# Kernel optimization log

Hardware: AMD Instinct MI355X
Metric: run time of the kernel (lower is better)

The kernel has to match this reference:

```python
import jax, jax.numpy as jnp
import numpy as np

TOP_K = 2


def setup_inputs() -> dict:
    key = jax.random.key(0)
    k1, k2, k3, k4 = jax.random.split(key, 4)
    B, S, H, I, E = 8, 2048, 768, 3072, 8
    x = jax.random.normal(k1, (B, S, H), dtype=jnp.float32)
    # kaiming_uniform-ish scale for weights
    router_w = jax.random.uniform(k2, (E, H), dtype=jnp.float32, minval=-1.0, maxval=1.0) * (1.0 / np.sqrt(H))
    up_w = jax.random.uniform(k3, (E, H, I), dtype=jnp.float32, minval=-1.0, maxval=1.0) * (1.0 / np.sqrt(H))
    down_w = jax.random.uniform(k4, (E, I, H), dtype=jnp.float32, minval=-1.0, maxval=1.0) * (1.0 / np.sqrt(I))
    return {"x": x, "router_w": router_w, "up_w": up_w, "down_w": down_w}


def reference(x, router_w, up_w, down_w):
    B, S, H = x.shape
    E = up_w.shape[0]
    T = B * S
    xf = x.reshape(T, H)
    # router: Linear(H -> E, bias=False) then softmax, top-k, renormalize
    logits = xf @ router_w.T                      # [T, E]
    probs = jax.nn.softmax(logits, axis=-1)
    top_w, top_i = jax.lax.top_k(probs, TOP_K)    # [T, K]
    top_w = top_w / jnp.sum(top_w, axis=-1, keepdims=True)
    # dense per-(token, expert) gate: zero for unselected experts
    gate = jnp.zeros((T, E), dtype=xf.dtype).at[jnp.arange(T)[:, None], top_i].add(top_w)
    # combine: sum_e gate[:, e] * down_e(gelu(up_e(x)))
    out = jnp.zeros_like(xf)
    for e in range(E):  # fixed small expert count; loop is structural, not over data dims
        h = jax.nn.gelu(xf @ up_w[e], approximate=False)   # exact GELU == torch F.gelu
        out = out + gate[:, e:e + 1] * (h @ down_w[e])
    return out.reshape(B, S, H)
```

## Files before the change

kernel.cpp:

```cpp
#include <hip/hip_runtime.h>

typedef short bf16x8 __attribute__((ext_vector_type(8)));
typedef float f32x4  __attribute__((ext_vector_type(4)));

#define T_TOK 16384
#define HD 768
#define ID 3072
#define NE 8
#define NT1MAX 136

__device__ __forceinline__ unsigned short f2bf(float f) {
    unsigned int u = __float_as_uint(f);
    unsigned int r = (u + 0x7FFFu + ((u >> 16) & 1u)) >> 16;
    return (unsigned short)r;
}

__device__ __forceinline__ void gload16(const void* g, void* l) {
    __builtin_amdgcn_global_load_lds(
        (const __attribute__((address_space(1))) void*)g,
        (__attribute__((address_space(3))) void*)l, 16, 0, 0);
}

__device__ __forceinline__ float gelu_f(float x) {
    float z = fabsf(x) * 0.70710678118f;
    float t = 1.0f / fmaf(0.3275911f, z, 1.0f);
    float p = t * fmaf(t, fmaf(t, fmaf(t, fmaf(t, 1.061405429f, -1.453152027f),
                                       1.421413741f), -0.284496736f), 0.254829592f);
    float e = 1.0f - p * __expf(-z * z);
    float erfv = (x >= 0.f) ? e : -e;
    return 0.5f * x * (1.0f + erfv);
}

__device__ __forceinline__ int xcd_swz(int bid, int nwg) {
    int q = nwg >> 3, rr = nwg & 7;
    int xcd = bid & 7, seq = bid >> 3;
    return (xcd < rr ? xcd * (q + 1) : rr * (q + 1) + (xcd - rr) * q) + seq;
}

__global__ __launch_bounds__(256) void k_cvt_x(const float* __restrict__ x,
                                               unsigned short* __restrict__ xb) {
    int i = blockIdx.x * 256 + threadIdx.x;
    float4 v = ((const float4*)x)[i];
    ushort4 o;
    o.x = f2bf(v.x); o.y = f2bf(v.y); o.z = f2bf(v.z); o.w = f2bf(v.w);
    ((ushort4*)xb)[i] = o;
}

__global__ __launch_bounds__(256) void k_tp(const float* __restrict__ in,
                                            unsigned short* __restrict__ out,
                                            int R, int C) {
    __shared__ float t[64][65];
    const float* ine = in + (size_t)blockIdx.z * R * C;
    unsigned short* oute = out + (size_t)blockIdx.z * R * C;
    int c0 = blockIdx.x * 64, r0 = blockIdx.y * 64;
    int lc = threadIdx.x & 63, lr4 = threadIdx.x >> 6;
#pragma unroll
    for (int i = 0; i < 16; i++) {
        int r = i * 4 + lr4;
        t[r][lc] = ine[(size_t)(r0 + r) * C + c0 + lc];
    }
    __syncthreads();
#pragma unroll
    for (int i = 0; i < 16; i++) {
        int r = i * 4 + lr4;
        oute[(size_t)(c0 + r) * R + r0 + lc] = f2bf(t[lc][r]);
    }
}

__global__ __launch_bounds__(256) void k_router(const float* __restrict__ x,
                                                const float* __restrict__ rw,
                                                int* __restrict__ topE,
                                                float* __restrict__ topW) {
    __shared__ float lrw[NE * HD];
    for (int i = threadIdx.x; i < NE * HD; i += 256) lrw[i] = rw[i];
    __syncthreads();
    int lane = threadIdx.x & 63;
    int t = blockIdx.x * 4 + (threadIdx.x >> 6);
    const float* xr = x + (size_t)t * HD;
    float acc[NE] = {0, 0, 0, 0, 0, 0, 0, 0};
    for (int h = lane; h < HD; h += 64) {
        float xv = xr[h];
#pragma unroll
        for (int e = 0; e < NE; e++) acc[e] = fmaf(xv, lrw[e * HD + h], acc[e]);
    }
#pragma unroll
    for (int e = 0; e < NE; e++) {
        float v = acc[e];
#pragma unroll
        for (int o = 32; o > 0; o >>= 1) v += __shfl_xor(v, o, 64);
        acc[e] = v;
    }
    if (lane == 0) {
        int e1 = 0; float l1 = acc[0];
#pragma unroll
        for (int e = 1; e < NE; e++) if (acc[e] > l1) { l1 = acc[e]; e1 = e; }
        int e2 = -1; float l2 = -1e30f;
#pragma unroll
        for (int e = 0; e < NE; e++) if (e != e1 && acc[e] > l2) { l2 = acc[e]; e2 = e; }
        float ex = expf(l2 - l1);
        float w1 = 1.0f / (1.0f + ex);
        topE[2 * t] = e1; topE[2 * t + 1] = e2;
        topW[2 * t] = w1; topW[2 * t + 1] = ex * w1;
    }
}

__global__ __launch_bounds__(256) void k_scatter(const int* __restrict__ topE,
                                                 const float* __restrict__ topW,
                                                 int* __restrict__ counts,
                                                 int* __restrict__ tokL,
                                                 float* __restrict__ gateL) {
    __shared__ int lc[NE], lbase[NE];
    if (threadIdx.x < NE) lc[threadIdx.x] = 0;
    __syncthreads();
    int t = blockIdx.x * 256 + threadIdx.x;
    int e1 = topE[2 * t], e2 = topE[2 * t + 1];
    int p1 = atomicAdd(&lc[e1], 1);
    int p2 = atomicAdd(&lc[e2], 1);
    __syncthreads();
    if (threadIdx.x < NE) lbase[threadIdx.x] = atomicAdd(&counts[threadIdx.x], lc[threadIdx.x]);
    __syncthreads();
    int q1 = lbase[e1] + p1, q2 = lbase[e2] + p2;
    tokL[e1 * T_TOK + q1] = t;  gateL[e1 * T_TOK + q1] = topW[2 * t];
    tokL[e2 * T_TOK + q2] = t;  gateL[e2 * T_TOK + q2] = topW[2 * t + 1];
}

__global__ void k_desc(const int* __restrict__ counts, int* __restrict__ tileE,
                       int* __restrict__ tileM0) {
    if (threadIdx.x == 0 && blockIdx.x == 0) {
        int tl = 0;
        for (int e = 0; e < NE; e++) {
            int c = counts[e];
            int nt = (c + 255) >> 8;
            for (int t = 0; t < nt; t++) { tileE[tl] = e; tileM0[tl] = t << 8; tl++; }
        }
        for (; tl < NT1MAX; tl++) { tileE[tl] = -1; tileM0[tl] = 0; }
    }
}

__global__ __launch_bounds__(512, 2) void k_gemm1(
    const unsigned short* __restrict__ xb,
    const unsigned short* __restrict__ upt,
    const int* __restrict__ tokL,
    const int* __restrict__ counts,
    const int* __restrict__ tileE,
    const int* __restrict__ tileM0,
    unsigned short* __restrict__ h,
    int seg, int ntn, int ldh) {
    __shared__ __align__(16) char lds[4][32768];
    constexpr int NK = HD / 32;
    int L = xcd_swz(blockIdx.x, gridDim.x);
    int mt = L / ntn, ntl = L - mt * ntn;
    int e = tileE[mt];
    if (e < 0) return;
    int m0 = tileM0[mt];
    int nrow = min(256, counts[e] - m0);
    const int* tok = tokL + e * T_TOK + m0;
    int n0 = (seg * ntn + ntl) * 256;

    const int tid = threadIdx.x, lane = tid & 63, wid = tid >> 6;
    const int wm = wid >> 2, wn = wid & 3;
    const int g = lane >> 4, r = lane & 15;

    int ar0 = wid * 16 + r;
    int ar1 = 128 + wid * 16 + r;
    const char* a0 = (const char*)(xb + (size_t)tok[ar0 < nrow ? ar0 : 0] * HD);
    const char* a1 = (const char*)(xb + (size_t)tok[ar1 < nrow ? ar1 : 0] * HD);
    const char* bsl = (const char*)(upt + (size_t)e * ID * HD);
    const char* b0 = bsl + (size_t)(n0 + wid * 16 + r) * (HD * 2);
    const char* b1 = bsl + (size_t)(n0 + 128 + wid * 16 + r) * (HD * 2);
    const int dst = wid * 1024;
    const int koff = g * 16;

    auto issue = [&](int step, int slot) {
        char* base = &lds[slot][0];
        int kb = step * 64 + koff;
        gload16(a0 + kb, base + dst);
        gload16(a1 + kb, base + 8192 + dst);
        gload16(b0 + kb, base + 16384 + dst);
        gload16(b1 + kb, base + 24576 + dst);
    };

    f32x4 acc[8][4];
#pragma unroll
    for (int m = 0; m < 8; m++)
#pragma unroll
        for (int n = 0; n < 4; n++) acc[m][n] = (f32x4){0.f, 0.f, 0.f, 0.f};

    issue(0, 0); issue(1, 1); issue(2, 2);
    asm volatile("s_waitcnt vmcnt(8)" ::: "memory");
    __builtin_amdgcn_s_barrier();
    asm volatile("" ::: "memory");

    const int aoff = wm * 8192 + g * 256 + r * 16;
    const int boff = 16384 + wn * 4096 + g * 256 + r * 16;

    for (int k = 0; k < NK; k++) {
        char* base = &lds[k & 3][0];
        bf16x8 a[4], b[4];
#pragma unroll
        for (int n = 0; n < 4; n++) b[n] = *(const bf16x8*)(base + boff + n * 1024);
#pragma unroll
        for (int m = 0; m < 4; m++) a[m] = *(const bf16x8*)(base + aoff + m * 1024);
        issue(min(k + 3, NK - 1), (k + 3) & 3);
        __builtin_amdgcn_s_setprio(1);
#pragma unroll
        for (int m = 0; m < 4; m++)
#pragma unroll
            for (int n = 0; n < 4; n++)
                acc[m][n] = __builtin_amdgcn_mfma_f32_16x16x32_bf16(a[m], b[n], acc[m][n], 0, 0, 0);
        __builtin_amdgcn_s_setprio(0);
#pragma unroll
        for (int m = 0; m < 4; m++) a[m] = *(const bf16x8*)(base + aoff + (4 + m) * 1024);
        __builtin_amdgcn_s_setprio(1);
#pragma unroll
        for (int m = 0; m < 4; m++)
#pragma unroll
            for (int n = 0; n < 4; n++)
                acc[4 + m][n] = __builtin_amdgcn_mfma_f32_16x16x32_bf16(a[m], b[n], acc[4 + m][n], 0, 0, 0);
        __builtin_amdgcn_s_setprio(0);
        asm volatile("s_waitcnt vmcnt(8)" ::: "memory");
        __builtin_amdgcn_s_barrier();
        asm volatile("" ::: "memory");
    }
    asm volatile("s_waitcnt vmcnt(0)" ::: "memory");

#pragma unroll
    for (int m = 0; m < 8; m++)
#pragma unroll
        for (int j = 0; j < 4; j++) {
            int rl = wm * 128 + m * 16 + g * 4 + j;
            if (rl < nrow) {
                unsigned short* hr = h + (size_t)(mt * 256 + rl) * ldh + ntl * 256 + wn * 64 + r;
#pragma unroll
                for (int n = 0; n < 4; n++) hr[n * 16] = f2bf(gelu_f(acc[m][n][j]));
            }
        }
}

__global__ __launch_bounds__(512, 2) void k_gemm2(
    const unsigned short* __restrict__ h,
    const unsigned short* __restrict__ dnt,
    const int* __restrict__ tokL,
    const float* __restrict__ gateL,
    const int* __restrict__ counts,
    const int* __restrict__ tileE,
    const int* __restrict__ tileM0,
    float* __restrict__ out,
    int seg, int ldh, int nk) {
    __shared__ __align__(16) char lds[4][32768];
    int L = xcd_swz(blockIdx.x, gridDim.x);
    int mt = L / 3, ntl = L - mt * 3;
    int e = tileE[mt];
    if (e < 0) return;
    int m0 = tileM0[mt];
    int nrow = min(256, counts[e] - m0);
    const int* tok = tokL + e * T_TOK + m0;
    const float* gat = gateL + e * T_TOK + m0;
    int n0 = ntl * 256;

    const int tid = threadIdx.x, lane = tid & 63, wid = tid >> 6;
    const int wm = wid >> 2, wn = wid & 3;
    const int g = lane >> 4, r = lane & 15;

    int ar0 = wid * 16 + r;
    int ar1 = 128 + wid * 16 + r;
    const char* a0 = (const char*)h + ((size_t)(mt * 256 + ar0) * ldh) * 2;
    const char* a1 = (const char*)h + ((size_t)(mt * 256 + ar1) * ldh) * 2;
    const char* bsl = (const char*)(dnt + (size_t)e * ID * HD) + (size_t)seg * ldh * 2;
    const char* b0 = bsl + (size_t)(n0 + wid * 16 + r) * (ID * 2);
    const char* b1 = bsl + (size_t)(n0 + 128 + wid * 16 + r) * (ID * 2);
    const int dst = wid * 1024;
    const int koff = g * 16;

    auto issue = [&](int step, int slot) {
        char* base = &lds[slot][0];
        int kb = step * 64 + koff;
        gload16(a0 + kb, base + dst);
        gload16(a1 + kb, base + 8192 + dst);
        gload16(b0 + kb, base + 16384 + dst);
        gload16(b1 + kb, base + 24576 + dst);
    };

    f32x4 acc[8][4];
#pragma unroll
    for (int m = 0; m < 8; m++)
#pragma unroll
        for (int n = 0; n < 4; n++) acc[m][n] = (f32x4){0.f, 0.f, 0.f, 0.f};

    issue(0, 0); issue(1, 1); issue(2, 2);
    asm volatile("s_waitcnt vmcnt(8)" ::: "memory");
    __builtin_amdgcn_s_barrier();
    asm volatile("" ::: "memory");

    const int aoff = wm * 8192 + g * 256 + r * 16;
    const int boff = 16384 + wn * 4096 + g * 256 + r * 16;

    for (int k = 0; k < nk; k++) {
        char* base = &lds[k & 3][0];
        bf16x8 a[4], b[4];
#pragma unroll
        for (int n = 0; n < 4; n++) b[n] = *(const bf16x8*)(base + boff + n * 1024);
#pragma unroll
        for (int m = 0; m < 4; m++) a[m] = *(const bf16x8*)(base + aoff + m * 1024);
        issue(min(k + 3, nk - 1), (k + 3) & 3);
        __builtin_amdgcn_s_setprio(1);
#pragma unroll
        for (int m = 0; m < 4; m++)
#pragma unroll
            for (int n = 0; n < 4; n++)
                acc[m][n] = __builtin_amdgcn_mfma_f32_16x16x32_bf16(a[m], b[n], acc[m][n], 0, 0, 0);
        __builtin_amdgcn_s_setprio(0);
#pragma unroll
        for (int m = 0; m < 4; m++) a[m] = *(const bf16x8*)(base + aoff + (4 + m) * 1024);
        __builtin_amdgcn_s_setprio(1);
#pragma unroll
        for (int m = 0; m < 4; m++)
#pragma unroll
            for (int n = 0; n < 4; n++)
                acc[4 + m][n] = __builtin_amdgcn_mfma_f32_16x16x32_bf16(a[m], b[n], acc[4 + m][n], 0, 0, 0);
        __builtin_amdgcn_s_setprio(0);
        asm volatile("s_waitcnt vmcnt(8)" ::: "memory");
        __builtin_amdgcn_s_barrier();
        asm volatile("" ::: "memory");
    }
    asm volatile("s_waitcnt vmcnt(0)" ::: "memory");

#pragma unroll
    for (int m = 0; m < 8; m++)
#pragma unroll
        for (int j = 0; j < 4; j++) {
            int rl = wm * 128 + m * 16 + g * 4 + j;
            if (rl < nrow) {
                int t = tok[rl];
                float gv = gat[rl];
                float* orow = out + (size_t)t * HD + n0 + wn * 64 + r;
#pragma unroll
                for (int n = 0; n < 4; n++)
                    atomicAdd(orow + n * 16, gv * acc[m][n][j]);
            }
        }
}

__global__ __launch_bounds__(512, 2) void k_moe(
    const unsigned short* __restrict__ xb,
    const unsigned short* __restrict__ upt,
    const unsigned short* __restrict__ dnt,
    const int* __restrict__ counts,
    const int* __restrict__ tokL,
    const float* __restrict__ gateL,
    float* __restrict__ out) {
    __shared__ __align__(16) char lds[155648];
    char* xs = lds;
    char* hs = lds + 98304;
    char* ring = lds + 106496;

    const int e = blockIdx.x & 7;
    const int slot = blockIdx.x >> 3;
    const int cnt = counts[e];
    if (slot * 64 >= cnt) return;
    const int nrow = min(64, cnt - slot * 64);
    const int* tok = tokL + e * T_TOK + slot * 64;
    const float* gat = gateL + e * T_TOK + slot * 64;

    const int tid = threadIdx.x;
    const int lane = tid & 63;
    const int wid = tid >> 6;
    const int mi = wid >> 2, ni = wid & 3;

    const char* upe = (const char*)(upt + (size_t)e * ID * HD);
    const char* dne = (const char*)(dnt + (size_t)e * HD * ID);

    {
        int off = tid * 16;
#pragma unroll
        for (int s = 0; s < 12; s++) {
            int o = off + s * 8192;
            int m = o / 1536;
            int cb = o - m * 1536;
            int tk = (m < nrow) ? tok[m] : tok[0];
            const char* src = (const char*)xb + (size_t)tk * 1536 + (size_t)(cb ^ ((m & 7) << 4));
            gload16(src, xs + s * 8192 + wid * 1024);
        }
    }
    asm volatile("s_waitcnt vmcnt(0)" ::: "memory");
    __builtin_amdgcn_s_barrier();
    asm volatile("" ::: "memory");

    auto issue = [&](int s) {
        char* dst = ring + (s % 6) * 8192 + wid * 1024;
        int ci = s / 24;
        int ph = s - ci * 24;
        int row = tid >> 3;
        int cb = (tid & 7) << 4;
        int scb = cb ^ ((row & 7) << 4);
        const char* src;
        if (ci >= 48) src = upe;
        else if (ph < 12) src = upe + (size_t)(ci * 64 + row) * 1536 + ph * 128 + scb;
        else              src = dne + (size_t)((ph - 12) * 64 + row) * 6144 + ci * 128 + scb;
        gload16(src, dst);
    };

    f32x4 acc[2][12];
#pragma unroll
    for (int a = 0; a < 2; a++)
#pragma unroll
        for (int b = 0; b < 12; b++) acc[a][b] = (f32x4){0.f, 0.f, 0.f, 0.f};

    issue(0); issue(1); issue(2); issue(3);

    f32x4 acch[2];
    bf16x8 ha[2][2];

    for (int ci = 0; ci < 48; ci++) {
#pragma unroll
        for (int ks = 0; ks < 12; ks++) {
            issue(ci * 24 + ks + 4);
            asm volatile("s_waitcnt vmcnt(4)" ::: "memory");
            __builtin_amdgcn_s_barrier();
            asm volatile("" ::: "memory");
            char* buf = ring + (ks % 6) * 8192;
            if (ks == 0) { acch[0] = (f32x4){0.f,0.f,0.f,0.f}; acch[1] = (f32x4){0.f,0.f,0.f,0.f}; }
#pragma unroll
            for (int kr = 0; kr < 2; kr++) {
                int bn = ni * 16 + (lane & 15);
                int bo = ((kr * 32 + (lane >> 4) * 8) * 2) ^ ((bn & 7) << 4);
                bf16x8 bfrag = *(const bf16x8*)(buf + bn * 128 + bo);
#pragma unroll
                for (int mr = 0; mr < 2; mr++) {
                    int ar = mi * 32 + mr * 16 + (lane & 15);
                    int ao = ((ks * 64 + kr * 32 + (lane >> 4) * 8) * 2) ^ ((ar & 7) << 4);
                    bf16x8 afrag = *(const bf16x8*)(xs + ar * 1536 + ao);
                    acch[mr] = __builtin_amdgcn_mfma_f32_16x16x32_bf16(afrag, bfrag, acch[mr], 0, 0, 0);
                }
            }
            if (ks == 11) {
#pragma unroll
                for (int mr = 0; mr < 2; mr++) {
                    int col = ni * 16 + (lane & 15);
#pragma unroll
                    for (int r = 0; r < 4; r++) {
                        int m = mi * 32 + mr * 16 + (lane >> 4) * 4 + r;
                        float v = acch[mr][r];
                        *(unsigned short*)(hs + m * 128 + ((col * 2) ^ ((m & 7) << 4))) = f2bf(gelu_f(v));
                    }
                }
                asm volatile("s_waitcnt lgkmcnt(0)" ::: "memory");
            }
        }
#pragma unroll
        for (int j = 0; j < 12; j++) {
            issue(ci * 24 + 12 + j + 4);
            asm volatile("s_waitcnt vmcnt(4)" ::: "memory");
            __builtin_amdgcn_s_barrier();
            asm volatile("" ::: "memory");
            char* buf = ring + ((12 + j) % 6) * 8192;
            if (j == 0) {
#pragma unroll
                for (int mr = 0; mr < 2; mr++)
#pragma unroll
                    for (int kr = 0; kr < 2; kr++) {
                        int ar = mi * 32 + mr * 16 + (lane & 15);
                        int ao = ((kr * 32 + (lane >> 4) * 8) * 2) ^ ((ar & 7) << 4);
                        ha[mr][kr] = *(const bf16x8*)(hs + ar * 128 + ao);
                    }
            }
#pragma unroll
            for (int kr = 0; kr < 2; kr++) {
                int bn = ni * 16 + (lane & 15);
                int bo = ((kr * 32 + (lane >> 4) * 8) * 2) ^ ((bn & 7) << 4);
                bf16x8 bfrag = *(const bf16x8*)(buf + bn * 128 + bo);
#pragma unroll
                for (int mr = 0; mr < 2; mr++)
                    acc[mr][j] = __builtin_amdgcn_mfma_f32_16x16x32_bf16(ha[mr][kr], bfrag, acc[mr][j], 0, 0, 0);
            }
        }
    }

    int   t4[2][4];
    float g4[2][4];
#pragma unroll
    for (int mr = 0; mr < 2; mr++)
#pragma unroll
        for (int r = 0; r < 4; r++) {
            int m = mi * 32 + mr * 16 + (lane >> 4) * 4 + r;
            bool valid = m < nrow;
            t4[mr][r] = valid ? tok[m] : -1;
            g4[mr][r] = valid ? gat[m] : 0.f;
        }
#pragma unroll
    for (int mr = 0; mr < 2; mr++)
#pragma unroll
        for (int j = 0; j < 12; j++) {
            int colg = j * 64 + ni * 16 + (lane & 15);
#pragma unroll
            for (int r = 0; r < 4; r++) {
                if (t4[mr][r] >= 0)
                    atomicAdd(out + (size_t)t4[mr][r] * HD + colg, g4[mr][r] * acc[mr][j][r]);
            }
        }
}

extern "C" void kernel_launch(void* const* d_in, const int* in_sizes, int n_in,
                              void* d_out, int out_size, void* d_ws, size_t ws_size,
                              hipStream_t stream) {
    const float* x  = (const float*)d_in[0];
    const float* rw = (const float*)d_in[1];
    const float* uw = (const float*)d_in[2];
    const float* dw = (const float*)d_in[3];
    float* out = (float*)d_out;

    size_t off = 0;
    char* base = (char*)d_ws;
    auto alloc = [&](size_t bytes) -> char* {
        char* p = base + off;
        off += (bytes + 1023) & ~(size_t)1023;
        return p;
    };
    unsigned short* xb   = (unsigned short*)alloc((size_t)T_TOK * HD * 2);
    unsigned short* upt  = (unsigned short*)alloc((size_t)NE * ID * HD * 2);
    unsigned short* dnt  = (unsigned short*)alloc((size_t)NE * HD * ID * 2);
    int*   topE   = (int*)alloc((size_t)T_TOK * 2 * 4);
    float* topW   = (float*)alloc((size_t)T_TOK * 2 * 4);
    int*   counts = (int*)alloc(256);
    int*   tileE  = (int*)alloc(NT1MAX * 4);
    int*   tileM0 = (int*)alloc(NT1MAX * 4);
    int*   tokL   = (int*)alloc((size_t)NE * T_TOK * 4);
    float* gateL  = (float*)alloc((size_t)NE * T_TOK * 4);
    size_t fixed = off;

    const int cand[6] = {1, 2, 3, 4, 6, 12};
    int S = 0;
    size_t hrows = (size_t)NT1MAX * 256;
    for (int i = 0; i < 6; i++) {
        size_t hb = hrows * (ID / cand[i]) * 2;
        if (fixed + hb <= ws_size) { S = cand[i]; break; }
    }
    unsigned short* h = (unsigned short*)(base + fixed);

    hipMemsetAsync(d_out, 0, (size_t)T_TOK * HD * 4, stream);
    hipMemsetAsync(counts, 0, 256, stream);

    k_cvt_x<<<(T_TOK * HD) / (256 * 4), 256, 0, stream>>>(x, xb);
    k_tp<<<dim3(ID / 64, HD / 64, NE), 256, 0, stream>>>(uw, upt, HD, ID);
    k_tp<<<dim3(HD / 64, ID / 64, NE), 256, 0, stream>>>(dw, dnt, ID, HD);
    k_router<<<T_TOK / 4, 256, 0, stream>>>(x, rw, topE, topW);
    k_scatter<<<T_TOK / 256, 256, 0, stream>>>(topE, topW, counts, tokL, gateL);

    if (S > 0) {
        int ntn = 12 / S;
        int ldh = ID / S;
        int nk2 = ldh / 32;
        k_desc<<<1, 64, 0, stream>>>(counts, tileE, tileM0);
        for (int sg = 0; sg < S; sg++) {
            k_gemm1<<<NT1MAX * ntn, 512, 0, stream>>>(xb, upt, tokL, counts, tileE, tileM0,
                                                      h, sg, ntn, ldh);
            k_gemm2<<<NT1MAX * 3, 512, 0, stream>>>(h, dnt, tokL, gateL, counts, tileE, tileM0,
                                                    out, sg, ldh, nk2);
        }
    } else {
        k_moe<<<2048, 512, 0, stream>>>(xb, upt, dnt, counts, tokL, gateL, out);
    }
}
```

Baseline: 775.6 us.

## Deepen GEMM LDS pipeline to five stages and fuse x conversion into router

Both grouped GEMM kernels move from a 4-slot to a 5-slot LDS ring, prefetching four steps ahead with matching vmcnt waits. Launch bounds drop to one block per CU to make room for the larger LDS footprint. The separate fp32-to-bf16 conversion kernel for x is folded into the router kernel, which saves one launch and one full read pass over x. The deeper prefetch is meant to hide more global-load latency, at the cost of halving occupancy per CU.

```diff
diff --git a/kernel.cpp b/kernel.cpp
--- a/kernel.cpp
+++ b/kernel.cpp
@@ -37,15 +37,6 @@
     return (xcd < rr ? xcd * (q + 1) : rr * (q + 1) + (xcd - rr) * q) + seq;
 }
 
-__global__ __launch_bounds__(256) void k_cvt_x(const float* __restrict__ x,
-                                               unsigned short* __restrict__ xb) {
-    int i = blockIdx.x * 256 + threadIdx.x;
-    float4 v = ((const float4*)x)[i];
-    ushort4 o;
-    o.x = f2bf(v.x); o.y = f2bf(v.y); o.z = f2bf(v.z); o.w = f2bf(v.w);
-    ((ushort4*)xb)[i] = o;
-}
-
 __global__ __launch_bounds__(256) void k_tp(const float* __restrict__ in,
                                             unsigned short* __restrict__ out,
                                             int R, int C) {
@@ -69,10 +60,22 @@
 
 __global__ __launch_bounds__(256) void k_router(const float* __restrict__ x,
                                                 const float* __restrict__ rw,
+                                                unsigned short* __restrict__ xb,
                                                 int* __restrict__ topE,
                                                 float* __restrict__ topW) {
     __shared__ float lrw[NE * HD];
     for (int i = threadIdx.x; i < NE * HD; i += 256) lrw[i] = rw[i];
+    {
+        const float4* xs4 = (const float4*)(x + (size_t)blockIdx.x * 4 * HD);
+        ushort4* xb4 = (ushort4*)(xb + (size_t)blockIdx.x * 4 * HD);
+#pragma unroll
+        for (int i = 0; i < 3; i++) {
+            float4 v = xs4[threadIdx.x + i * 256];
+            ushort4 o;
+            o.x = f2bf(v.x); o.y = f2bf(v.y); o.z = f2bf(v.z); o.w = f2bf(v.w);
+            xb4[threadIdx.x + i * 256] = o;
+        }
+    }
     __syncthreads();
     int lane = threadIdx.x & 63;
     int t = blockIdx.x * 4 + (threadIdx.x >> 6);
@@ -137,7 +140,7 @@
     }
 }
 
-__global__ __launch_bounds__(512, 2) void k_gemm1(
+__global__ __launch_bounds__(512, 1) void k_gemm1(
     const unsigned short* __restrict__ xb,
     const unsigned short* __restrict__ upt,
     const int* __restrict__ tokL,
@@ -146,7 +149,7 @@
     const int* __restrict__ tileM0,
     unsigned short* __restrict__ h,
     int seg, int ntn, int ldh) {
-    __shared__ __align__(16) char lds[4][32768];
+    __shared__ __align__(16) char lds[5][32768];
     constexpr int NK = HD / 32;
     int L = xcd_swz(blockIdx.x, gridDim.x);
     int mt = L / ntn, ntl = L - mt * ntn;
@@ -163,17 +166,16 @@
 
     int ar0 = wid * 16 + r;
     int ar1 = 128 + wid * 16 + r;
-    const char* a0 = (const char*)(xb + (size_t)tok[ar0 < nrow ? ar0 : 0] * HD);
-    const char* a1 = (const char*)(xb + (size_t)tok[ar1 < nrow ? ar1 : 0] * HD);
+    const char* a0 = (const char*)(xb + (size_t)tok[ar0 < nrow ? ar0 : 0] * HD) + g * 16;
+    const char* a1 = (const char*)(xb + (size_t)tok[ar1 < nrow ? ar1 : 0] * HD) + g * 16;
     const char* bsl = (const char*)(upt + (size_t)e * ID * HD);
-    const char* b0 = bsl + (size_t)(n0 + wid * 16 + r) * (HD * 2);
-    const char* b1 = bsl + (size_t)(n0 + 128 + wid * 16 + r) * (HD * 2);
+    const char* b0 = bsl + (size_t)(n0 + wid * 16 + r) * (HD * 2) + g * 16;
+    const char* b1 = bsl + (size_t)(n0 + 128 + wid * 16 + r) * (HD * 2) + g * 16;
     const int dst = wid * 1024;
-    const int koff = g * 16;
 
     auto issue = [&](int step, int slot) {
         char* base = &lds[slot][0];
-        int kb = step * 64 + koff;
+        int kb = step * 64;
         gload16(a0 + kb, base + dst);
         gload16(a1 + kb, base + 8192 + dst);
         gload16(b0 + kb, base + 16384 + dst);
@@ -186,8 +188,8 @@
 #pragma unroll
         for (int n = 0; n < 4; n++) acc[m][n] = (f32x4){0.f, 0.f, 0.f, 0.f};
 
-    issue(0, 0); issue(1, 1); issue(2, 2);
-    asm volatile("s_waitcnt vmcnt(8)" ::: "memory");
+    issue(0, 0); issue(1, 1); issue(2, 2); issue(3, 3);
+    asm volatile("s_waitcnt vmcnt(12)" ::: "memory");
     __builtin_amdgcn_s_barrier();
     asm volatile("" ::: "memory");
 
@@ -195,13 +197,13 @@
     const int boff = 16384 + wn * 4096 + g * 256 + r * 16;
 
     for (int k = 0; k < NK; k++) {
-        char* base = &lds[k & 3][0];
+        char* base = &lds[k % 5][0];
         bf16x8 a[4], b[4];
 #pragma unroll
         for (int n = 0; n < 4; n++) b[n] = *(const bf16x8*)(base + boff + n * 1024);
 #pragma unroll
         for (int m = 0; m < 4; m++) a[m] = *(const bf16x8*)(base + aoff + m * 1024);
-        issue(min(k + 3, NK - 1), (k + 3) & 3);
+        issue(min(k + 4, NK - 1), (k + 4) % 5);
         __builtin_amdgcn_s_setprio(1);
 #pragma unroll
         for (int m = 0; m < 4; m++)
@@ -218,7 +220,7 @@
             for (int n = 0; n < 4; n++)
                 acc[4 + m][n] = __builtin_amdgcn_mfma_f32_16x16x32_bf16(a[m], b[n], acc[4 + m][n], 0, 0, 0);
         __builtin_amdgcn_s_setprio(0);
-        asm volatile("s_waitcnt vmcnt(8)" ::: "memory");
+        asm volatile("s_waitcnt vmcnt(12)" ::: "memory");
         __builtin_amdgcn_s_barrier();
         asm volatile("" ::: "memory");
     }
@@ -237,7 +239,7 @@
         }
 }
 
-__global__ __launch_bounds__(512, 2) void k_gemm2(
+__global__ __launch_bounds__(512, 1) void k_gemm2(
     const unsigned short* __restrict__ h,
     const unsigned short* __restrict__ dnt,
     const int* __restrict__ tokL,
@@ -247,7 +249,7 @@
     const int* __restrict__ tileM0,
     float* __restrict__ out,
     int seg, int ldh, int nk) {
-    __shared__ __align__(16) char lds[4][32768];
+    __shared__ __align__(16) char lds[5][32768];
     int L = xcd_swz(blockIdx.x, gridDim.x);
     int mt = L / 3, ntl = L - mt * 3;
     int e = tileE[mt];
@@ -264,17 +266,16 @@
 
     int ar0 = wid * 16 + r;
     int ar1 = 128 + wid * 16 + r;
-    const char* a0 = (const char*)h + ((size_t)(mt * 256 + ar0) * ldh) * 2;
-    const char* a1 = (const char*)h + ((size_t)(mt * 256 + ar1) * ldh) * 2;
+    const char* a0 = (const char*)h + ((size_t)(mt * 256 + ar0) * ldh) * 2 + g * 16;
+    const char* a1 = (const char*)h + ((size_t)(mt * 256 + ar1) * ldh) * 2 + g * 16;
     const char* bsl = (const char*)(dnt + (size_t)e * ID * HD) + (size_t)seg * ldh * 2;
-    const char* b0 = bsl + (size_t)(n0 + wid * 16 + r) * (ID * 2);
-    const char* b1 = bsl + (size_t)(n0 + 128 + wid * 16 + r) * (ID * 2);
+    const char* b0 = bsl + (size_t)(n0 + wid * 16 + r) * (ID * 2) + g * 16;
+    const char* b1 = bsl + (size_t)(n0 + 128 + wid * 16 + r) * (ID * 2) + g * 16;
     const int dst = wid * 1024;
-    const int koff = g * 16;
 
     auto issue = [&](int step, int slot) {
         char* base = &lds[slot][0];
-        int kb = step * 64 + koff;
+        int kb = step * 64;
         gload16(a0 + kb, base + dst);
         gload16(a1 + kb, base + 8192 + dst);
         gload16(b0 + kb, base + 16384 + dst);
@@ -287,8 +288,8 @@
 #pragma unroll
         for (int n = 0; n < 4; n++) acc[m][n] = (f32x4){0.f, 0.f, 0.f, 0.f};
 
-    issue(0, 0); issue(1, 1); issue(2, 2);
-    asm volatile("s_waitcnt vmcnt(8)" ::: "memory");
+    issue(0, 0); issue(1, 1); issue(2, 2); issue(3, 3);
+    asm volatile("s_waitcnt vmcnt(12)" ::: "memory");
     __builtin_amdgcn_s_barrier();
     asm volatile("" ::: "memory");
 
@@ -296,13 +297,13 @@
     const int boff = 16384 + wn * 4096 + g * 256 + r * 16;
 
     for (int k = 0; k < nk; k++) {
-        char* base = &lds[k & 3][0];
+        char* base = &lds[k % 5][0];
         bf16x8 a[4], b[4];
 #pragma unroll
         for (int n = 0; n < 4; n++) b[n] = *(const bf16x8*)(base + boff + n * 1024);
 #pragma unroll
         for (int m = 0; m < 4; m++) a[m] = *(const bf16x8*)(base + aoff + m * 1024);
-        issue(min(k + 3, nk - 1), (k + 3) & 3);
+        issue(min(k + 4, nk - 1), (k + 4) % 5);
         __builtin_amdgcn_s_setprio(1);
 #pragma unroll
         for (int m = 0; m < 4; m++)
@@ -319,7 +320,7 @@
             for (int n = 0; n < 4; n++)
                 acc[4 + m][n] = __builtin_amdgcn_mfma_f32_16x16x32_bf16(a[m], b[n], acc[4 + m][n], 0, 0, 0);
         __builtin_amdgcn_s_setprio(0);
-        asm volatile("s_waitcnt vmcnt(8)" ::: "memory");
+        asm volatile("s_waitcnt vmcnt(12)" ::: "memory");
         __builtin_amdgcn_s_barrier();
         asm volatile("" ::: "memory");
     }
@@ -387,7 +388,7 @@
     asm volatile("" ::: "memory");
 
     auto issue = [&](int s) {
-        char* dst = ring + (s % 6) * 8192 + wid * 1024;
+        char* dstp = ring + (s % 6) * 8192 + wid * 1024;
         int ci = s / 24;
         int ph = s - ci * 24;
         int row = tid >> 3;
@@ -397,7 +398,7 @@
         if (ci >= 48) src = upe;
         else if (ph < 12) src = upe + (size_t)(ci * 64 + row) * 1536 + ph * 128 + scb;
         else              src = dne + (size_t)((ph - 12) * 64 + row) * 6144 + ci * 128 + scb;
-        gload16(src, dst);
+        gload16(src, dstp);
     };
 
     f32x4 acc[2][12];
@@ -421,14 +422,14 @@
             char* buf = ring + (ks % 6) * 8192;
             if (ks == 0) { acch[0] = (f32x4){0.f,0.f,0.f,0.f}; acch[1] = (f32x4){0.f,0.f,0.f,0.f}; }
 #pragma unroll
-            for (int kr = 0; kr < 2; kr++) {
+            for (int kkr = 0; kkr < 2; kkr++) {
                 int bn = ni * 16 + (lane & 15);
-                int bo = ((kr * 32 + (lane >> 4) * 8) * 2) ^ ((bn & 7) << 4);
+                int bo = ((kkr * 32 + (lane >> 4) * 8) * 2) ^ ((bn & 7) << 4);
                 bf16x8 bfrag = *(const bf16x8*)(buf + bn * 128 + bo);
 #pragma unroll
                 for (int mr = 0; mr < 2; mr++) {
                     int ar = mi * 32 + mr * 16 + (lane & 15);
-                    int ao = ((ks * 64 + kr * 32 + (lane >> 4) * 8) * 2) ^ ((ar & 7) << 4);
+                    int ao = ((ks * 64 + kkr * 32 + (lane >> 4) * 8) * 2) ^ ((ar & 7) << 4);
                     bf16x8 afrag = *(const bf16x8*)(xs + ar * 1536 + ao);
                     acch[mr] = __builtin_amdgcn_mfma_f32_16x16x32_bf16(afrag, bfrag, acch[mr], 0, 0, 0);
                 }
@@ -438,9 +439,9 @@
                 for (int mr = 0; mr < 2; mr++) {
                     int col = ni * 16 + (lane & 15);
 #pragma unroll
-                    for (int r = 0; r < 4; r++) {
-                        int m = mi * 32 + mr * 16 + (lane >> 4) * 4 + r;
-                        float v = acch[mr][r];
+                    for (int rr = 0; rr < 4; rr++) {
+                        int m = mi * 32 + mr * 16 + (lane >> 4) * 4 + rr;
+                        float v = acch[mr][rr];
                         *(unsigned short*)(hs + m * 128 + ((col * 2) ^ ((m & 7) << 4))) = f2bf(gelu_f(v));
                     }
                 }
@@ -458,20 +459,20 @@
 #pragma unroll
                 for (int mr = 0; mr < 2; mr++)
 #pragma unroll
-                    for (int kr = 0; kr < 2; kr++) {
+                    for (int kkr = 0; kkr < 2; kkr++) {
                         int ar = mi * 32 + mr * 16 + (lane & 15);
-                        int ao = ((kr * 32 + (lane >> 4) * 8) * 2) ^ ((ar & 7) << 4);
-                        ha[mr][kr] = *(const bf16x8*)(hs + ar * 128 + ao);
+                        int ao = ((kkr * 32 + (lane >> 4) * 8) * 2) ^ ((ar & 7) << 4);
+                        ha[mr][kkr] = *(const bf16x8*)(hs + ar * 128 + ao);
                     }
             }
 #pragma unroll
-            for (int kr = 0; kr < 2; kr++) {
+            for (int kkr = 0; kkr < 2; kkr++) {
                 int bn = ni * 16 + (lane & 15);
-                int bo = ((kr * 32 + (lane >> 4) * 8) * 2) ^ ((bn & 7) << 4);
+                int bo = ((kkr * 32 + (lane >> 4) * 8) * 2) ^ ((bn & 7) << 4);
                 bf16x8 bfrag = *(const bf16x8*)(buf + bn * 128 + bo);
 #pragma unroll
                 for (int mr = 0; mr < 2; mr++)
-                    acc[mr][j] = __builtin_amdgcn_mfma_f32_16x16x32_bf16(ha[mr][kr], bfrag, acc[mr][j], 0, 0, 0);
+                    acc[mr][j] = __builtin_amdgcn_mfma_f32_16x16x32_bf16(ha[mr][kkr], bfrag, acc[mr][j], 0, 0, 0);
             }
         }
     }
@@ -481,11 +482,11 @@
 #pragma unroll
     for (int mr = 0; mr < 2; mr++)
 #pragma unroll
-        for (int r = 0; r < 4; r++) {
-            int m = mi * 32 + mr * 16 + (lane >> 4) * 4 + r;
+        for (int rr = 0; rr < 4; rr++) {
+            int m = mi * 32 + mr * 16 + (lane >> 4) * 4 + rr;
             bool valid = m < nrow;
-            t4[mr][r] = valid ? tok[m] : -1;
-            g4[mr][r] = valid ? gat[m] : 0.f;
+            t4[mr][rr] = valid ? tok[m] : -1;
+            g4[mr][rr] = valid ? gat[m] : 0.f;
         }
 #pragma unroll
     for (int mr = 0; mr < 2; mr++)
@@ -493,9 +494,9 @@
         for (int j = 0; j < 12; j++) {
             int colg = j * 64 + ni * 16 + (lane & 15);
 #pragma unroll
-            for (int r = 0; r < 4; r++) {
-                if (t4[mr][r] >= 0)
-                    atomicAdd(out + (size_t)t4[mr][r] * HD + colg, g4[mr][r] * acc[mr][j][r]);
+            for (int rr = 0; rr < 4; rr++) {
+                if (t4[mr][rr] >= 0)
+                    atomicAdd(out + (size_t)t4[mr][rr] * HD + colg, g4[mr][rr] * acc[mr][j][rr]);
             }
         }
 }
@@ -540,15 +541,14 @@
     hipMemsetAsync(d_out, 0, (size_t)T_TOK * HD * 4, stream);
     hipMemsetAsync(counts, 0, 256, stream);
 
-    k_cvt_x<<<(T_TOK * HD) / (256 * 4), 256, 0, stream>>>(x, xb);
     k_tp<<<dim3(ID / 64, HD / 64, NE), 256, 0, stream>>>(uw, upt, HD, ID);
     k_tp<<<dim3(HD / 64, ID / 64, NE), 256, 0, stream>>>(dw, dnt, ID, HD);
-    k_router<<<T_TOK / 4, 256, 0, stream>>>(x, rw, topE, topW);
+    k_router<<<T_TOK / 4, 256, 0, stream>>>(x, rw, xb, topE, topW);
     k_scatter<<<T_TOK / 256, 256, 0, stream>>>(topE, topW, counts, tokL, gateL);
 
     if (S > 0) {
-        int ntn = 12 / S;
         int ldh = ID / S;
+        int ntn = ldh / 256;
         int nk2 = ldh / 32;
         k_desc<<<1, 64, 0, stream>>>(counts, tileE, tileM0);
         for (int sg = 0; sg < S; sg++) {
```

Result: faster. 754.9 us (-2.7%).
